# Optimization experiments

Measured on AMD Instinct MI355X. Metric: run time of the kernel, lower is better.

## Reference

```python
import jax, jax.numpy as jnp
import numpy as np

N_NODES = 50000
N_EDGES = 800000


def setup_inputs() -> dict:
    key = jax.random.key(0)
    ks = jax.random.split(key, 9)
    d, h, hd = 128, 4, 32
    s = 1.0 / np.sqrt(d)
    return {
        "x": jax.random.normal(ks[0], (N_NODES, d), jnp.float32),
        "edge_index": jax.random.randint(ks[1], (2, N_EDGES), 0, N_NODES, jnp.int32),
        "W0": jax.random.normal(ks[2], (d, d), jnp.float32) * s,
        "att_l0": jax.random.normal(ks[3], (h, hd), jnp.float32) * s,
        "att_r0": jax.random.normal(ks[4], (h, hd), jnp.float32) * s,
        "b0": jnp.zeros((d,), jnp.float32),
        "W1": jax.random.normal(ks[5], (d, d), jnp.float32) * s,
        "att_l1": jax.random.normal(ks[6], (h, hd), jnp.float32) * s,
        "att_r1": jax.random.normal(ks[7], (h, hd), jnp.float32) * s,
        "b1": jnp.zeros((hd,), jnp.float32),
    }


def _gat_layer(x, src, dst, W, att_l, att_r, bias, concat):
    # x: [N, F_in]; W: [H*D, F_in] (torch Linear layout); att_*: [H, D]
    n = x.shape[0]
    h, d = att_l.shape
    hx = (x @ W.T).reshape(n, h, d)                     # [N,H,D]
    al = jnp.einsum('nhd,hd->nh', hx, att_l)            # [N,H]
    ar = jnp.einsum('nhd,hd->nh', hx, att_r)
    att = al[src] + ar[dst]                             # [E,H]
    att = jax.nn.leaky_relu(att, negative_slope=0.2)
    # segment softmax over destination nodes
    m = jax.ops.segment_max(att, dst, num_segments=n)   # [N,H]
    att = jnp.exp(att - m[dst])
    ssum = jax.ops.segment_sum(att, dst, num_segments=n)
    att = att / (ssum[dst] + 1e-9)                      # [E,H]
    msgs = att[:, :, None] * hx[src]                    # [E,H,D]
    out = jax.ops.segment_sum(msgs, dst, num_segments=n)  # [N,H,D]
    if concat:
        out = out.reshape(n, h * d)
    else:
        out = out.mean(axis=1)
    return out + bias


def reference(x, edge_index, W0, att_l0, att_r0, b0, W1, att_l1, att_r1, b1):
    src, dst = edge_index[0], edge_index[1]
    x = _gat_layer(x, src, dst, W0, att_l0, att_r0, b0, concat=True)
    x = jax.nn.relu(x)  # dropout is identity in eval mode
    x = _gat_layer(x, src, dst, W1, att_l1, att_r1, b1, concat=False)
    return x
```

## Files before the change

kernel.cpp:

```cpp
#include <hip/hip_runtime.h>
#include <hip/hip_bf16.h>

#define H 4
#define D 32
#define F 128
#define MAXDEG 64
#define DEGSTRIDE 16

typedef __attribute__((ext_vector_type(8))) short bf16x8;
typedef __attribute__((ext_vector_type(4))) float f32x4;

__device__ __forceinline__ short f2bf(float v) {
    __hip_bfloat16 h = __float2bfloat16(v);
    return *reinterpret_cast<short*>(&h);
}
__device__ __forceinline__ float bf2f(short s) {
    __hip_bfloat16 h = *reinterpret_cast<__hip_bfloat16*>(&s);
    return __bfloat162float(h);
}

__device__ __forceinline__
void gemm_body(int bid, int nblocks, const float* __restrict__ X,
               const float* __restrict__ W, const float* __restrict__ attl,
               const float* __restrict__ attr, __hip_bfloat16* __restrict__ HXB,
               float* __restrict__ AL, float* __restrict__ AR, int ntiles) {
    const int wave = threadIdx.x >> 6;
    const int lane = threadIdx.x & 63;
    const int m    = lane & 15;
    const int q    = lane >> 4;
    const int q8   = q * 8;

    bf16x8 Bhi[2][4], Blo[2][4];
#pragma unroll
    for (int j = 0; j < 2; ++j) {
        const int fout = wave * 32 + j * 16 + m;
#pragma unroll
        for (int kc = 0; kc < 4; ++kc) {
            const float* wp = W + (size_t)fout * F + kc * 32 + q8;
            float4 w0 = *reinterpret_cast<const float4*>(wp);
            float4 w1 = *reinterpret_cast<const float4*>(wp + 4);
            float wv[8] = {w0.x, w0.y, w0.z, w0.w, w1.x, w1.y, w1.z, w1.w};
#pragma unroll
            for (int t = 0; t < 8; ++t) {
                short h = f2bf(wv[t]);
                Bhi[j][kc][t] = h;
                Blo[j][kc][t] = f2bf(wv[t] - bf2f(h));
            }
        }
    }
    const float alw0  = attl[wave * 32 + m];
    const float alw16 = attl[wave * 32 + 16 + m];
    const float arw0  = attr[wave * 32 + m];
    const float arw16 = attr[wave * 32 + 16 + m];

    for (int tile = bid; tile < ntiles; tile += nblocks) {
        const int node0 = tile * 16;
        bf16x8 Ahi[4], Alo[4];
        const float* xp = X + (size_t)(node0 + m) * F + q8;
#pragma unroll
        for (int kc = 0; kc < 4; ++kc) {
            float4 x0 = *reinterpret_cast<const float4*>(xp + kc * 32);
            float4 x1 = *reinterpret_cast<const float4*>(xp + kc * 32 + 4);
            float xv[8] = {x0.x, x0.y, x0.z, x0.w, x1.x, x1.y, x1.z, x1.w};
#pragma unroll
            for (int t = 0; t < 8; ++t) {
                short h = f2bf(xv[t]);
                Ahi[kc][t] = h;
                Alo[kc][t] = f2bf(xv[t] - bf2f(h));
            }
        }
        f32x4 acc0 = {0.f, 0.f, 0.f, 0.f};
        f32x4 acc1 = {0.f, 0.f, 0.f, 0.f};
#pragma unroll
        for (int kc = 0; kc < 4; ++kc) {
            acc0 = __builtin_amdgcn_mfma_f32_16x16x32_bf16(Ahi[kc], Bhi[0][kc], acc0, 0, 0, 0);
            acc1 = __builtin_amdgcn_mfma_f32_16x16x32_bf16(Ahi[kc], Bhi[1][kc], acc1, 0, 0, 0);
            acc0 = __builtin_amdgcn_mfma_f32_16x16x32_bf16(Ahi[kc], Blo[0][kc], acc0, 0, 0, 0);
            acc1 = __builtin_amdgcn_mfma_f32_16x16x32_bf16(Ahi[kc], Blo[1][kc], acc1, 0, 0, 0);
            acc0 = __builtin_amdgcn_mfma_f32_16x16x32_bf16(Alo[kc], Bhi[0][kc], acc0, 0, 0, 0);
            acc1 = __builtin_amdgcn_mfma_f32_16x16x32_bf16(Alo[kc], Bhi[1][kc], acc1, 0, 0, 0);
        }
        const int row0 = node0 + q * 4;
        const int col0 = wave * 32 + m;
#pragma unroll
        for (int r = 0; r < 4; ++r) {
            HXB[(size_t)(row0 + r) * F + col0]      = __float2bfloat16(acc0[r]);
            HXB[(size_t)(row0 + r) * F + col0 + 16] = __float2bfloat16(acc1[r]);
            float pal = acc0[r] * alw0 + acc1[r] * alw16;
            float par = acc0[r] * arw0 + acc1[r] * arw16;
#pragma unroll
            for (int o = 1; o < 16; o <<= 1) {
                pal += __shfl_xor(pal, o);
                par += __shfl_xor(par, o);
            }
            if (m == 0) {
                AL[(size_t)(row0 + r) * H + wave] = pal;
                AR[(size_t)(row0 + r) * H + wave] = par;
            }
        }
    }
}

__device__ __forceinline__
void scatter_body(int bid, const int* __restrict__ ei, int E,
                  int* __restrict__ deg16, int* __restrict__ ssrc2) {
    int base = (bid * 256 + (int)threadIdx.x) * 4;
    if (base + 3 < E) {
        int4 src4 = *reinterpret_cast<const int4*>(ei + base);
        int4 dst4 = *reinterpret_cast<const int4*>(ei + E + base);
        int s0 = atomicAdd(&deg16[dst4.x * DEGSTRIDE], 1);
        int s1 = atomicAdd(&deg16[dst4.y * DEGSTRIDE], 1);
        int s2 = atomicAdd(&deg16[dst4.z * DEGSTRIDE], 1);
        int s3 = atomicAdd(&deg16[dst4.w * DEGSTRIDE], 1);
        if (s0 < MAXDEG) ssrc2[dst4.x * MAXDEG + s0] = src4.x;
        if (s1 < MAXDEG) ssrc2[dst4.y * MAXDEG + s1] = src4.y;
        if (s2 < MAXDEG) ssrc2[dst4.z * MAXDEG + s2] = src4.z;
        if (s3 < MAXDEG) ssrc2[dst4.w * MAXDEG + s3] = src4.w;
    } else {
        for (int e = base; e < E; ++e) {
            int src = ei[e], dst = ei[E + e];
            int s = atomicAdd(&deg16[dst * DEGSTRIDE], 1);
            if (s < MAXDEG) ssrc2[dst * MAXDEG + s] = src;
        }
    }
}

__global__ __launch_bounds__(256)
void k_gemm_scatter(const float* __restrict__ X, const float* __restrict__ W,
                    const float* __restrict__ attl, const float* __restrict__ attr,
                    __hip_bfloat16* __restrict__ HXB, float* __restrict__ AL,
                    float* __restrict__ AR, int ntiles, int gemm_blocks,
                    const int* __restrict__ ei, int E,
                    int* __restrict__ deg16, int* __restrict__ ssrc2) {
    if ((int)blockIdx.x < gemm_blocks)
        gemm_body(blockIdx.x, gemm_blocks, X, W, attl, attr, HXB, AL, AR, ntiles);
    else
        scatter_body(blockIdx.x - gemm_blocks, ei, E, deg16, ssrc2);
}

__global__ __launch_bounds__(256)
void k_gemm(const float* __restrict__ X, const float* __restrict__ W,
            const float* __restrict__ attl, const float* __restrict__ attr,
            __hip_bfloat16* __restrict__ HXB, float* __restrict__ AL,
            float* __restrict__ AR, int ntiles) {
    gemm_body(blockIdx.x, gridDim.x, X, W, attl, attr, HXB, AL, AR, ntiles);
}

template<int MODE>
__global__ __launch_bounds__(256)
void k_aggr(const int* __restrict__ ssrc2, const int* __restrict__ deg16,
            const float* __restrict__ AL, const float* __restrict__ AR,
            const __hip_bfloat16* __restrict__ HXB, const float* __restrict__ bias,
            float* __restrict__ out, int N) {
    __shared__ int   sidx[4][MAXDEG];
    __shared__ float sw[4][MAXDEG][H];
    const int g = threadIdx.x >> 6;
    const int t = threadIdx.x & 63;
    const int n = blockIdx.x * 4 + g;
    if (n >= N) return;
    const int h = t >> 4;
    const int cnt = min(deg16[n * DEGSTRIDE], MAXDEG);
    const float4 ar4 = *reinterpret_cast<const float4*>(AR + (size_t)n * H);
    if (t < cnt) {
        int s = ssrc2[n * MAXDEG + t];
        sidx[g][t] = s;
        float4 al4 = *reinterpret_cast<const float4*>(AL + (size_t)s * H);
        float a0 = al4.x + ar4.x; a0 = a0 > 0.f ? a0 : 0.2f * a0;
        float a1 = al4.y + ar4.y; a1 = a1 > 0.f ? a1 : 0.2f * a1;
        float a2 = al4.z + ar4.z; a2 = a2 > 0.f ? a2 : 0.2f * a2;
        float a3 = al4.w + ar4.w; a3 = a3 > 0.f ? a3 : 0.2f * a3;
        sw[g][t][0] = __expf(a0);
        sw[g][t][1] = __expf(a1);
        sw[g][t][2] = __expf(a2);
        sw[g][t][3] = __expf(a3);
    }
    __builtin_amdgcn_wave_barrier();
    float accx = 0.f, accy = 0.f, wsum = 0.f;
    int e = 0;
    for (; e + 4 <= cnt; e += 4) {
        int s0 = sidx[g][e], s1 = sidx[g][e + 1], s2 = sidx[g][e + 2], s3 = sidx[g][e + 3];
        float w0 = sw[g][e][h], w1 = sw[g][e + 1][h], w2 = sw[g][e + 2][h], w3 = sw[g][e + 3][h];
        float2 f0 = __bfloat1622float2(*reinterpret_cast<const __hip_bfloat162*>(HXB + (size_t)s0 * F + 2 * t));
        float2 f1 = __bfloat1622float2(*reinterpret_cast<const __hip_bfloat162*>(HXB + (size_t)s1 * F + 2 * t));
        float2 f2 = __bfloat1622float2(*reinterpret_cast<const __hip_bfloat162*>(HXB + (size_t)s2 * F + 2 * t));
        float2 f3 = __bfloat1622float2(*reinterpret_cast<const __hip_bfloat162*>(HXB + (size_t)s3 * F + 2 * t));
        accx += w0 * f0.x + w1 * f1.x + w2 * f2.x + w3 * f3.x;
        accy += w0 * f0.y + w1 * f1.y + w2 * f2.y + w3 * f3.y;
        wsum += (w0 + w1) + (w2 + w3);
    }
    for (; e < cnt; ++e) {
        int s = sidx[g][e];
        float w = sw[g][e][h];
        float2 fv = __bfloat1622float2(*reinterpret_cast<const __hip_bfloat162*>(HXB + (size_t)s * F + 2 * t));
        accx += w * fv.x;
        accy += w * fv.y;
        wsum += w;
    }
    float inv = 1.f / (wsum + 1e-9f);
    float vx = accx * inv, vy = accy * inv;
    if (MODE == 0) {
        float2 o;
        o.x = fmaxf(vx + bias[2 * t], 0.f);
        o.y = fmaxf(vy + bias[2 * t + 1], 0.f);
        *reinterpret_cast<float2*>(out + (size_t)n * F + 2 * t) = o;
    } else {
        vx += __shfl_xor(vx, 16); vx += __shfl_xor(vx, 32);
        vy += __shfl_xor(vy, 16); vy += __shfl_xor(vy, 32);
        if (t < 16) {
            float2 o;
            o.x = 0.25f * vx + bias[2 * t];
            o.y = 0.25f * vy + bias[2 * t + 1];
            *reinterpret_cast<float2*>(out + (size_t)n * D + 2 * t) = o;
        }
    }
}

extern "C" void kernel_launch(void* const* d_in, const int* in_sizes, int n_in,
                              void* d_out, int out_size, void* d_ws, size_t ws_size,
                              hipStream_t stream) {
    const float* x     = (const float*)d_in[0];
    const int*   ei    = (const int*)d_in[1];
    const float* W0    = (const float*)d_in[2];
    const float* attl0 = (const float*)d_in[3];
    const float* attr0 = (const float*)d_in[4];
    const float* b0    = (const float*)d_in[5];
    const float* W1    = (const float*)d_in[6];
    const float* attl1 = (const float*)d_in[7];
    const float* attr1 = (const float*)d_in[8];
    const float* b1    = (const float*)d_in[9];

    const int N = in_sizes[0] / F;
    const int E = in_sizes[1] / 2;
    const int ntiles = N / 16;

    char* p = (char*)d_ws;
    __hip_bfloat16* HXB = (__hip_bfloat16*)p;  p += (size_t)N * F * 2;
    float* X1  = (float*)p;                    p += (size_t)N * F * 4;
    float* AL  = (float*)p;                    p += (size_t)N * H * 4;
    float* AR  = (float*)p;                    p += (size_t)N * H * 4;
    int* ssrc2 = (int*)p;                      p += (size_t)N * MAXDEG * 4;
    int* deg16 = (int*)p;                      p += (size_t)N * DEGSTRIDE * 4;

    hipMemsetAsync(deg16, 0, (size_t)N * DEGSTRIDE * sizeof(int), stream);

    const int gemm_blocks    = 625;
    const int scatter_blocks = (E / 4 + 255) / 256;
    const int aggr_blocks    = (N + 3) / 4;

    k_gemm_scatter<<<gemm_blocks + scatter_blocks, 256, 0, stream>>>(
        x, W0, attl0, attr0, HXB, AL, AR, ntiles, gemm_blocks, ei, E, deg16, ssrc2);
    k_aggr<0><<<aggr_blocks, 256, 0, stream>>>(ssrc2, deg16, AL, AR, HXB, b0, X1, N);

    k_gemm<<<gemm_blocks, 256, 0, stream>>>(X1, W1, attl1, attr1, HXB, AL, AR, ntiles);
    k_aggr<1><<<aggr_blocks, 256, 0, stream>>>(ssrc2, deg16, AL, AR, HXB, b1, (float*)d_out, N);
}
```

Measured before the change: 235.8 us.

## Fuse layer-0 aggregation with layer-1 GEMM and compact edge scatter

Layer-0 aggregation now writes each 16-node tile into shared memory, and the same block immediately runs the layer-1 projection on MFMA using a split-bf16 (hi/lo) weight, so the fp32 X1 intermediate never goes to HBM and one launch is removed. W1 is pre-split into bf16 hi/lo in the first kernel. The edge scatter is partitioned into 8 destination ranges selected by blockIdx&7 to localise atomics, and source indices are stored as 16-bit values to halve the adjacency buffer. The trade-offs: edge_index is read 8 times, and the ushort indices only work when N fits in 65536.

```diff
diff --git a/kernel.cpp b/kernel.cpp
--- a/kernel.cpp
+++ b/kernel.cpp
@@ -102,56 +102,205 @@
 }
 
 __device__ __forceinline__
-void scatter_body(int bid, const int* __restrict__ ei, int E,
-                  int* __restrict__ deg16, int* __restrict__ ssrc2) {
-    int base = (bid * 256 + (int)threadIdx.x) * 4;
-    if (base + 3 < E) {
-        int4 src4 = *reinterpret_cast<const int4*>(ei + base);
-        int4 dst4 = *reinterpret_cast<const int4*>(ei + E + base);
-        int s0 = atomicAdd(&deg16[dst4.x * DEGSTRIDE], 1);
-        int s1 = atomicAdd(&deg16[dst4.y * DEGSTRIDE], 1);
-        int s2 = atomicAdd(&deg16[dst4.z * DEGSTRIDE], 1);
-        int s3 = atomicAdd(&deg16[dst4.w * DEGSTRIDE], 1);
-        if (s0 < MAXDEG) ssrc2[dst4.x * MAXDEG + s0] = src4.x;
-        if (s1 < MAXDEG) ssrc2[dst4.y * MAXDEG + s1] = src4.y;
-        if (s2 < MAXDEG) ssrc2[dst4.z * MAXDEG + s2] = src4.z;
-        if (s3 < MAXDEG) ssrc2[dst4.w * MAXDEG + s3] = src4.w;
+void wconv_body(const float* __restrict__ W1, __hip_bfloat16* __restrict__ W1hi,
+                __hip_bfloat16* __restrict__ W1lo) {
+    for (int i = threadIdx.x; i < F * F; i += 256) {
+        float v = W1[i];
+        short hi = f2bf(v);
+        *reinterpret_cast<short*>(&W1hi[i]) = hi;
+        *reinterpret_cast<short*>(&W1lo[i]) = f2bf(v - bf2f(hi));
+    }
+}
+
+__device__ __forceinline__
+void scatter_body(int rawBid, int base, const int* __restrict__ ei, int E,
+                  int* __restrict__ deg16, unsigned short* __restrict__ ssrc2u,
+                  int per) {
+    const int c     = rawBid & 7;
+    const int strip = (rawBid - base) >> 3;
+    const int lo = c * per, hi = lo + per;
+    int ebase = strip * 1024 + (int)threadIdx.x * 4;
+    if (ebase >= E) return;
+    if (ebase + 3 < E) {
+        int4 s4 = *reinterpret_cast<const int4*>(ei + ebase);
+        int4 d4 = *reinterpret_cast<const int4*>(ei + E + ebase);
+        if (d4.x >= lo && d4.x < hi) {
+            int s = atomicAdd(&deg16[d4.x * DEGSTRIDE], 1);
+            if (s < MAXDEG) ssrc2u[d4.x * MAXDEG + s] = (unsigned short)s4.x;
+        }
+        if (d4.y >= lo && d4.y < hi) {
+            int s = atomicAdd(&deg16[d4.y * DEGSTRIDE], 1);
+            if (s < MAXDEG) ssrc2u[d4.y * MAXDEG + s] = (unsigned short)s4.y;
+        }
+        if (d4.z >= lo && d4.z < hi) {
+            int s = atomicAdd(&deg16[d4.z * DEGSTRIDE], 1);
+            if (s < MAXDEG) ssrc2u[d4.z * MAXDEG + s] = (unsigned short)s4.z;
+        }
+        if (d4.w >= lo && d4.w < hi) {
+            int s = atomicAdd(&deg16[d4.w * DEGSTRIDE], 1);
+            if (s < MAXDEG) ssrc2u[d4.w * MAXDEG + s] = (unsigned short)s4.w;
+        }
     } else {
-        for (int e = base; e < E; ++e) {
+        for (int e = ebase; e < E; ++e) {
             int src = ei[e], dst = ei[E + e];
-            int s = atomicAdd(&deg16[dst * DEGSTRIDE], 1);
-            if (s < MAXDEG) ssrc2[dst * MAXDEG + s] = src;
+            if (dst >= lo && dst < hi) {
+                int s = atomicAdd(&deg16[dst * DEGSTRIDE], 1);
+                if (s < MAXDEG) ssrc2u[dst * MAXDEG + s] = (unsigned short)src;
+            }
         }
     }
 }
 
 __global__ __launch_bounds__(256)
-void k_gemm_scatter(const float* __restrict__ X, const float* __restrict__ W,
-                    const float* __restrict__ attl, const float* __restrict__ attr,
-                    __hip_bfloat16* __restrict__ HXB, float* __restrict__ AL,
-                    float* __restrict__ AR, int ntiles, int gemm_blocks,
-                    const int* __restrict__ ei, int E,
-                    int* __restrict__ deg16, int* __restrict__ ssrc2) {
-    if ((int)blockIdx.x < gemm_blocks)
-        gemm_body(blockIdx.x, gemm_blocks, X, W, attl, attr, HXB, AL, AR, ntiles);
+void k_pre(const float* __restrict__ X, const float* __restrict__ W0,
+           const float* __restrict__ attl0, const float* __restrict__ attr0,
+           __hip_bfloat16* __restrict__ HXB0, float* __restrict__ AL0,
+           float* __restrict__ AR0, int ntiles, int gemm_blocks,
+           const float* __restrict__ W1, __hip_bfloat16* __restrict__ W1hi,
+           __hip_bfloat16* __restrict__ W1lo,
+           const int* __restrict__ ei, int E,
+           int* __restrict__ deg16, unsigned short* __restrict__ ssrc2u, int per) {
+    const int bid = blockIdx.x;
+    if (bid < gemm_blocks)
+        gemm_body(bid, gemm_blocks, X, W0, attl0, attr0, HXB0, AL0, AR0, ntiles);
+    else if (bid == gemm_blocks)
+        wconv_body(W1, W1hi, W1lo);
     else
-        scatter_body(blockIdx.x - gemm_blocks, ei, E, deg16, ssrc2);
+        scatter_body(bid, gemm_blocks + 1, ei, E, deg16, ssrc2u, per);
 }
 
 __global__ __launch_bounds__(256)
-void k_gemm(const float* __restrict__ X, const float* __restrict__ W,
-            const float* __restrict__ attl, const float* __restrict__ attr,
-            __hip_bfloat16* __restrict__ HXB, float* __restrict__ AL,
-            float* __restrict__ AR, int ntiles) {
-    gemm_body(blockIdx.x, gridDim.x, X, W, attl, attr, HXB, AL, AR, ntiles);
-}
-
-template<int MODE>
+void k_aggr_gemm(const unsigned short* __restrict__ ssrc2u, const int* __restrict__ deg16,
+                 const float* __restrict__ AL0, const float* __restrict__ AR0,
+                 const __hip_bfloat16* __restrict__ HXB0, const float* __restrict__ b0,
+                 const __hip_bfloat16* __restrict__ W1hi, const __hip_bfloat16* __restrict__ W1lo,
+                 const float* __restrict__ attl1, const float* __restrict__ attr1,
+                 __hip_bfloat16* __restrict__ HXB1, float* __restrict__ AL1,
+                 float* __restrict__ AR1) {
+    __shared__ float xs[16][132];
+    __shared__ int   sidx[4][MAXDEG];
+    __shared__ float sw[4][MAXDEG][H];
+    const int g = threadIdx.x >> 6;
+    const int t = threadIdx.x & 63;
+    const int h = t >> 4;
+    const int node0 = blockIdx.x * 16;
+
+    for (int i = 0; i < 4; ++i) {
+        const int n = node0 + g * 4 + i;
+        const int cnt = min(deg16[n * DEGSTRIDE], MAXDEG);
+        const float4 ar4 = *reinterpret_cast<const float4*>(AR0 + (size_t)n * H);
+        if (t < cnt) {
+            int s = ssrc2u[n * MAXDEG + t];
+            sidx[g][t] = s;
+            float4 al4 = *reinterpret_cast<const float4*>(AL0 + (size_t)s * H);
+            float a0 = al4.x + ar4.x; a0 = a0 > 0.f ? a0 : 0.2f * a0;
+            float a1 = al4.y + ar4.y; a1 = a1 > 0.f ? a1 : 0.2f * a1;
+            float a2 = al4.z + ar4.z; a2 = a2 > 0.f ? a2 : 0.2f * a2;
+            float a3 = al4.w + ar4.w; a3 = a3 > 0.f ? a3 : 0.2f * a3;
+            sw[g][t][0] = __expf(a0);
+            sw[g][t][1] = __expf(a1);
+            sw[g][t][2] = __expf(a2);
+            sw[g][t][3] = __expf(a3);
+        }
+        __builtin_amdgcn_wave_barrier();
+        float accx = 0.f, accy = 0.f, wsum = 0.f;
+        int e = 0;
+        for (; e + 4 <= cnt; e += 4) {
+            int s0 = sidx[g][e], s1 = sidx[g][e + 1], s2 = sidx[g][e + 2], s3 = sidx[g][e + 3];
+            float w0 = sw[g][e][h], w1 = sw[g][e + 1][h], w2 = sw[g][e + 2][h], w3 = sw[g][e + 3][h];
+            float2 f0 = __bfloat1622float2(*reinterpret_cast<const __hip_bfloat162*>(HXB0 + (size_t)s0 * F + 2 * t));
+            float2 f1 = __bfloat1622float2(*reinterpret_cast<const __hip_bfloat162*>(HXB0 + (size_t)s1 * F + 2 * t));
+            float2 f2 = __bfloat1622float2(*reinterpret_cast<const __hip_bfloat162*>(HXB0 + (size_t)s2 * F + 2 * t));
+            float2 f3 = __bfloat1622float2(*reinterpret_cast<const __hip_bfloat162*>(HXB0 + (size_t)s3 * F + 2 * t));
+            accx += w0 * f0.x + w1 * f1.x + w2 * f2.x + w3 * f3.x;
+            accy += w0 * f0.y + w1 * f1.y + w2 * f2.y + w3 * f3.y;
+            wsum += (w0 + w1) + (w2 + w3);
+        }
+        for (; e < cnt; ++e) {
+            int s = sidx[g][e];
+            float w = sw[g][e][h];
+            float2 fv = __bfloat1622float2(*reinterpret_cast<const __hip_bfloat162*>(HXB0 + (size_t)s * F + 2 * t));
+            accx += w * fv.x;
+            accy += w * fv.y;
+            wsum += w;
+        }
+        float inv = 1.f / (wsum + 1e-9f);
+        const int row = g * 4 + i;
+        xs[row][2 * t]     = fmaxf(accx * inv + b0[2 * t], 0.f);
+        xs[row][2 * t + 1] = fmaxf(accy * inv + b0[2 * t + 1], 0.f);
+        __builtin_amdgcn_wave_barrier();
+    }
+    __syncthreads();
+
+    const int wave = g;
+    const int m  = t & 15;
+    const int q  = t >> 4;
+    const int q8 = q * 8;
+
+    bf16x8 Bhi[2][4], Blo[2][4];
+#pragma unroll
+    for (int j = 0; j < 2; ++j) {
+        const int fout = wave * 32 + j * 16 + m;
+#pragma unroll
+        for (int kc = 0; kc < 4; ++kc) {
+            Bhi[j][kc] = *reinterpret_cast<const bf16x8*>(W1hi + (size_t)fout * F + kc * 32 + q8);
+            Blo[j][kc] = *reinterpret_cast<const bf16x8*>(W1lo + (size_t)fout * F + kc * 32 + q8);
+        }
+    }
+    bf16x8 Ahi[4], Alo[4];
+#pragma unroll
+    for (int kc = 0; kc < 4; ++kc) {
+        const float* xp = &xs[m][kc * 32 + q8];
+        float4 x0 = *reinterpret_cast<const float4*>(xp);
+        float4 x1 = *reinterpret_cast<const float4*>(xp + 4);
+        float xv[8] = {x0.x, x0.y, x0.z, x0.w, x1.x, x1.y, x1.z, x1.w};
+#pragma unroll
+        for (int u = 0; u < 8; ++u) {
+            short hi = f2bf(xv[u]);
+            Ahi[kc][u] = hi;
+            Alo[kc][u] = f2bf(xv[u] - bf2f(hi));
+        }
+    }
+    f32x4 acc0 = {0.f, 0.f, 0.f, 0.f};
+    f32x4 acc1 = {0.f, 0.f, 0.f, 0.f};
+#pragma unroll
+    for (int kc = 0; kc < 4; ++kc) {
+        acc0 = __builtin_amdgcn_mfma_f32_16x16x32_bf16(Ahi[kc], Bhi[0][kc], acc0, 0, 0, 0);
+        acc1 = __builtin_amdgcn_mfma_f32_16x16x32_bf16(Ahi[kc], Bhi[1][kc], acc1, 0, 0, 0);
+        acc0 = __builtin_amdgcn_mfma_f32_16x16x32_bf16(Ahi[kc], Blo[0][kc], acc0, 0, 0, 0);
+        acc1 = __builtin_amdgcn_mfma_f32_16x16x32_bf16(Ahi[kc], Blo[1][kc], acc1, 0, 0, 0);
+        acc0 = __builtin_amdgcn_mfma_f32_16x16x32_bf16(Alo[kc], Bhi[0][kc], acc0, 0, 0, 0);
+        acc1 = __builtin_amdgcn_mfma_f32_16x16x32_bf16(Alo[kc], Bhi[1][kc], acc1, 0, 0, 0);
+    }
+    const float alw0  = attl1[wave * 32 + m];
+    const float alw16 = attl1[wave * 32 + 16 + m];
+    const float arw0  = attr1[wave * 32 + m];
+    const float arw16 = attr1[wave * 32 + 16 + m];
+    const int row0 = node0 + q * 4;
+    const int col0 = wave * 32 + m;
+#pragma unroll
+    for (int r = 0; r < 4; ++r) {
+        HXB1[(size_t)(row0 + r) * F + col0]      = __float2bfloat16(acc0[r]);
+        HXB1[(size_t)(row0 + r) * F + col0 + 16] = __float2bfloat16(acc1[r]);
+        float pal = acc0[r] * alw0 + acc1[r] * alw16;
+        float par = acc0[r] * arw0 + acc1[r] * arw16;
+#pragma unroll
+        for (int o = 1; o < 16; o <<= 1) {
+            pal += __shfl_xor(pal, o);
+            par += __shfl_xor(par, o);
+        }
+        if (m == 0) {
+            AL1[(size_t)(row0 + r) * H + wave] = pal;
+            AR1[(size_t)(row0 + r) * H + wave] = par;
+        }
+    }
+}
+
 __global__ __launch_bounds__(256)
-void k_aggr(const int* __restrict__ ssrc2, const int* __restrict__ deg16,
-            const float* __restrict__ AL, const float* __restrict__ AR,
-            const __hip_bfloat16* __restrict__ HXB, const float* __restrict__ bias,
-            float* __restrict__ out, int N) {
+void k_aggr1(const unsigned short* __restrict__ ssrc2u, const int* __restrict__ deg16,
+             const float* __restrict__ AL, const float* __restrict__ AR,
+             const __hip_bfloat16* __restrict__ HXB, const float* __restrict__ bias,
+             float* __restrict__ out, int N) {
     __shared__ int   sidx[4][MAXDEG];
     __shared__ float sw[4][MAXDEG][H];
     const int g = threadIdx.x >> 6;
@@ -162,7 +311,7 @@
     const int cnt = min(deg16[n * DEGSTRIDE], MAXDEG);
     const float4 ar4 = *reinterpret_cast<const float4*>(AR + (size_t)n * H);
     if (t < cnt) {
-        int s = ssrc2[n * MAXDEG + t];
+        int s = ssrc2u[n * MAXDEG + t];
         sidx[g][t] = s;
         float4 al4 = *reinterpret_cast<const float4*>(AL + (size_t)s * H);
         float a0 = al4.x + ar4.x; a0 = a0 > 0.f ? a0 : 0.2f * a0;
@@ -198,20 +347,13 @@
     }
     float inv = 1.f / (wsum + 1e-9f);
     float vx = accx * inv, vy = accy * inv;
-    if (MODE == 0) {
+    vx += __shfl_xor(vx, 16); vx += __shfl_xor(vx, 32);
+    vy += __shfl_xor(vy, 16); vy += __shfl_xor(vy, 32);
+    if (t < 16) {
         float2 o;
-        o.x = fmaxf(vx + bias[2 * t], 0.f);
-        o.y = fmaxf(vy + bias[2 * t + 1], 0.f);
-        *reinterpret_cast<float2*>(out + (size_t)n * F + 2 * t) = o;
-    } else {
-        vx += __shfl_xor(vx, 16); vx += __shfl_xor(vx, 32);
-        vy += __shfl_xor(vy, 16); vy += __shfl_xor(vy, 32);
-        if (t < 16) {
-            float2 o;
-            o.x = 0.25f * vx + bias[2 * t];
-            o.y = 0.25f * vy + bias[2 * t + 1];
-            *reinterpret_cast<float2*>(out + (size_t)n * D + 2 * t) = o;
-        }
+        o.x = 0.25f * vx + bias[2 * t];
+        o.y = 0.25f * vy + bias[2 * t + 1];
+        *reinterpret_cast<float2*>(out + (size_t)n * D + 2 * t) = o;
     }
 }
 
@@ -232,25 +374,34 @@
     const int N = in_sizes[0] / F;
     const int E = in_sizes[1] / 2;
     const int ntiles = N / 16;
+    const int per = (N + 7) / 8;
 
     char* p = (char*)d_ws;
-    __hip_bfloat16* HXB = (__hip_bfloat16*)p;  p += (size_t)N * F * 2;
-    float* X1  = (float*)p;                    p += (size_t)N * F * 4;
-    float* AL  = (float*)p;                    p += (size_t)N * H * 4;
-    float* AR  = (float*)p;                    p += (size_t)N * H * 4;
-    int* ssrc2 = (int*)p;                      p += (size_t)N * MAXDEG * 4;
-    int* deg16 = (int*)p;                      p += (size_t)N * DEGSTRIDE * 4;
+    __hip_bfloat16* HXB0 = (__hip_bfloat16*)p;  p += (size_t)N * F * 2;
+    __hip_bfloat16* HXB1 = (__hip_bfloat16*)p;  p += (size_t)N * F * 2;
+    __hip_bfloat16* W1hi = (__hip_bfloat16*)p;  p += (size_t)F * F * 2;
+    __hip_bfloat16* W1lo = (__hip_bfloat16*)p;  p += (size_t)F * F * 2;
+    float* AL0 = (float*)p;                     p += (size_t)N * H * 4;
+    float* AR0 = (float*)p;                     p += (size_t)N * H * 4;
+    float* AL1 = (float*)p;                     p += (size_t)N * H * 4;
+    float* AR1 = (float*)p;                     p += (size_t)N * H * 4;
+    unsigned short* ssrc2u = (unsigned short*)p; p += (size_t)N * MAXDEG * 2;
+    int* deg16 = (int*)p;
 
     hipMemsetAsync(deg16, 0, (size_t)N * DEGSTRIDE * sizeof(int), stream);
 
-    const int gemm_blocks    = 625;
-    const int scatter_blocks = (E / 4 + 255) / 256;
-    const int aggr_blocks    = (N + 3) / 4;
-
-    k_gemm_scatter<<<gemm_blocks + scatter_blocks, 256, 0, stream>>>(
-        x, W0, attl0, attr0, HXB, AL, AR, ntiles, gemm_blocks, ei, E, deg16, ssrc2);
-    k_aggr<0><<<aggr_blocks, 256, 0, stream>>>(ssrc2, deg16, AL, AR, HXB, b0, X1, N);
-
-    k_gemm<<<gemm_blocks, 256, 0, stream>>>(X1, W1, attl1, attr1, HXB, AL, AR, ntiles);
-    k_aggr<1><<<aggr_blocks, 256, 0, stream>>>(ssrc2, deg16, AL, AR, HXB, b1, (float*)d_out, N);
-}
+    const int gemm_blocks = 625;
+    const int nstrips = (E + 1023) / 1024;
+    const int total_blocks = gemm_blocks + 1 + 8 * nstrips;
+
+    k_pre<<<total_blocks, 256, 0, stream>>>(x, W0, attl0, attr0, HXB0, AL0, AR0,
+                                            ntiles, gemm_blocks, W1, W1hi, W1lo,
+                                            ei, E, deg16, ssrc2u, per);
+
+    k_aggr_gemm<<<ntiles, 256, 0, stream>>>(ssrc2u, deg16, AL0, AR0, HXB0, b0,
+                                            W1hi, W1lo, attl1, attr1,
+                                            HXB1, AL1, AR1);
+
+    k_aggr1<<<(N + 3) / 4, 256, 0, stream>>>(ssrc2u, deg16, AL1, AR1, HXB1, b1,
+                                             (float*)d_out, N);
+}
```

After: 239.0 us. Within noise of the previous version (+1.4%).
